# Optimization experiments

Measured on AMD Instinct MI355X. Metric: run time of the kernel, lower is better.

Reference implementation:

```python
import jax, jax.numpy as jnp
import numpy as np

T, B = 128, 64
EMB, HID, NTOK = 400, 1152, 33278
# layer dims: (in, out) per layer, matching AWD_LSTM construction
LAYER_DIMS = [(EMB, HID), (HID, HID), (HID, EMB)]


def _uniform(key, shape, bound):
    return jax.random.uniform(key, shape, jnp.float32, -bound, bound)


def setup_inputs() -> dict:
    key = jax.random.key(0)
    ks = jax.random.split(key, 32)
    inp = {
        "x": jax.random.normal(ks[0], (T, B, EMB), jnp.float32),
        "h0_0": jnp.zeros((B, HID), jnp.float32),
        "h0_1": jnp.zeros((B, HID), jnp.float32),
        "h0_2": jnp.zeros((B, EMB), jnp.float32),
        "c0_0": jnp.zeros((B, HID), jnp.float32),
        "c0_1": jnp.zeros((B, HID), jnp.float32),
        "c0_2": jnp.zeros((B, EMB), jnp.float32),
    }
    ki = 1
    for li, (din, dout) in enumerate(LAYER_DIMS):
        bound = 1.0 / np.sqrt(dout)
        inp[f"W_ih{li}"] = _uniform(ks[ki + 0], (4 * dout, din), bound)
        inp[f"W_hh{li}"] = _uniform(ks[ki + 1], (4 * dout, dout), bound)
        inp[f"b_ih{li}"] = _uniform(ks[ki + 2], (4 * dout,), bound)
        inp[f"b_hh{li}"] = _uniform(ks[ki + 3], (4 * dout,), bound)
        ki += 4
    bd = 1.0 / np.sqrt(EMB)
    inp["W_dec"] = _uniform(ks[ki], (NTOK, EMB), bd)
    inp["b_dec"] = _uniform(ks[ki + 1], (NTOK,), bd)
    return inp


def _lstm_cell(x, h, c, W_ih, W_hh, b_ih, b_hh):
    # PyTorch gate order: i, f, g, o
    gates = x @ W_ih.T + b_ih + h @ W_hh.T + b_hh
    i, f, g, o = jnp.split(gates, 4, axis=-1)
    c_new = jax.nn.sigmoid(f) * c + jax.nn.sigmoid(i) * jnp.tanh(g)
    h_new = jax.nn.sigmoid(o) * jnp.tanh(c_new)
    return h_new, c_new


def reference(x, h0_0, h0_1, h0_2, c0_0, c0_1, c0_2,
              W_ih0, W_hh0, b_ih0, b_hh0,
              W_ih1, W_hh1, b_ih1, b_hh1,
              W_ih2, W_hh2, b_ih2, b_hh2,
              W_dec, b_dec):
    params = [(W_ih0, W_hh0, b_ih0, b_hh0),
              (W_ih1, W_hh1, b_ih1, b_hh1),
              (W_ih2, W_hh2, b_ih2, b_hh2)]

    def step(carry, xt):
        hs, cs = carry
        inp = xt
        new_h, new_c = [], []
        for li in range(3):
            h, c = _lstm_cell(inp, hs[li], cs[li], *params[li])
            new_h.append(h)
            new_c.append(c)
            inp = h
        return (tuple(new_h), tuple(new_c)), new_h[-1]

    carry0 = ((h0_0, h0_1, h0_2), (c0_0, c0_1, c0_2))
    (hs, cs), out = jax.lax.scan(step, carry0, x)  # out: (T, B, EMB)
    decoded = out.reshape(T * B, EMB) @ W_dec.T + b_dec
    return decoded.reshape(T, B, NTOK)
```

## Files before the change

kernel.cpp:

```cpp
#include <hip/hip_runtime.h>
#include <math.h>

typedef unsigned short u16;
typedef __attribute__((ext_vector_type(8))) short short8;
typedef __attribute__((ext_vector_type(4))) float f32x4;
typedef __attribute__((ext_vector_type(2))) float f32x2;

__device__ __forceinline__ u16 f32_to_bf16(float x) {
    union { float f; unsigned int u; } v; v.f = x;
    unsigned int u = v.u;
    return (u16)((u + 0x7FFFu + ((u >> 16) & 1u)) >> 16);
}
__device__ __forceinline__ float bf16_to_f32(u16 h) {
    union { unsigned int u; float f; } v; v.u = ((unsigned int)h) << 16; return v.f;
}

__global__ void split_pad_kernel(const float* __restrict__ src,
                                 u16* __restrict__ hi, u16* __restrict__ lo,
                                 int N, int K, int Npad, int Kpad, int perm)
{
    int idx = blockIdx.x * 256 + threadIdx.x;
    if (idx >= Npad * Kpad) return;
    int n = idx / Kpad, k = idx - n * Kpad;
    float x = 0.f;
    if (n < N && k < K) {
        int srow = n;
        if (perm) { int dout = N >> 2; srow = (n & 3) * dout + (n >> 2); }
        x = src[(size_t)srow * K + k];
    }
    u16 h = f32_to_bf16(x);
    hi[idx] = h;
    lo[idx] = f32_to_bf16(x - bf16_to_f32(h));
}

__global__ void bias_perm_kernel(const float* __restrict__ bi,
                                 const float* __restrict__ bh,
                                 float* __restrict__ out, int N4)
{
    int c = blockIdx.x * 256 + threadIdx.x;
    if (c >= N4) return;
    int dout = N4 >> 2;
    int s = (c & 3) * dout + (c >> 2);
    out[c] = bi[s] + bh[s];
}

__global__ __launch_bounds__(256) void gemm3m(
    const float* __restrict__ Af32,
    const u16* __restrict__ Ahi, const u16* __restrict__ Alo,
    const u16* __restrict__ Whi, const u16* __restrict__ Wlo,
    const float* __restrict__ bias,
    float* __restrict__ C,
    int Nreal, int Kreal, int Kp, int lda, int ldc, int amode,
    int MT, int NSUB)
{
    extern __shared__ __align__(16) char smem[];
    u16 (*As)[128][32] = (u16 (*)[128][32])smem;
    u16 (*Ws)[128][32] = (u16 (*)[128][32])(smem + 16384);
    float (*Cs)[129]   = (float (*)[129])smem;

    const int tid  = threadIdx.x;
    const int lane = tid & 63, wave = tid >> 6;

    const int bid   = blockIdx.x;
    const int super = bid / (NSUB * MT);
    const int rem   = bid - super * (NSUB * MT);
    const int mtile = rem / NSUB;
    const int ntile = super * NSUB + (rem - mtile * NSUB);
    const int m0 = mtile * 128, n0 = ntile * 128;

    const int wm = (wave >> 1) * 64, wn = (wave & 1) * 64;

    f32x4 acc[4][4];
#pragma unroll
    for (int i = 0; i < 4; ++i)
#pragma unroll
        for (int j = 0; j < 4; ++j)
#pragma unroll
            for (int r = 0; r < 4; ++r) acc[i][j][r] = 0.f;

    const int srow = tid >> 2;
    const int sq   = tid & 3;
    const int dq   = (sq ^ ((srow >> 2) & 3)) * 8;
    const int fr   = lane & 15;
    const int fq   = lane >> 4;
    const int rcol = (fq ^ ((fr >> 2) & 3)) * 8;

    for (int k0 = 0; k0 < Kp; k0 += 32) {
#pragma unroll
        for (int half = 0; half < 2; ++half) {
            int row = half * 64 + srow;
            int kc  = k0 + sq * 8;
            if (amode == 0) {
                union { u16 s[8]; short8 v; } uh, ul;
                if (kc + 8 <= Kreal) {
                    const float* p = &Af32[(size_t)(m0 + row) * lda + kc];
#pragma unroll
                    for (int j = 0; j < 8; ++j) {
                        float xv = p[j];
                        u16 hh = f32_to_bf16(xv);
                        uh.s[j] = hh;
                        ul.s[j] = f32_to_bf16(xv - bf16_to_f32(hh));
                    }
                } else {
#pragma unroll
                    for (int j = 0; j < 8; ++j) { uh.s[j] = 0; ul.s[j] = 0; }
                }
                *(short8*)&As[0][row][dq] = uh.v;
                *(short8*)&As[1][row][dq] = ul.v;
            } else {
                size_t ao = (size_t)(m0 + row) * lda + kc;
                *(short8*)&As[0][row][dq] = *(const short8*)(Ahi + ao);
                *(short8*)&As[1][row][dq] = *(const short8*)(Alo + ao);
            }
            size_t wo = (size_t)(n0 + row) * Kp + kc;
            *(short8*)&Ws[0][row][dq] = *(const short8*)(Whi + wo);
            *(short8*)&Ws[1][row][dq] = *(const short8*)(Wlo + wo);
        }
        __syncthreads();

        short8 ah[4], al[4], wh[4], wl[4];
#pragma unroll
        for (int f = 0; f < 4; ++f) {
            int arow = wm + f * 16 + fr;
            ah[f] = *(const short8*)&As[0][arow][rcol];
            al[f] = *(const short8*)&As[1][arow][rcol];
            int wrow = wn + f * 16 + fr;
            wh[f] = *(const short8*)&Ws[0][wrow][rcol];
            wl[f] = *(const short8*)&Ws[1][wrow][rcol];
        }
#pragma unroll
        for (int i = 0; i < 4; ++i)
#pragma unroll
            for (int j = 0; j < 4; ++j) {
                acc[i][j] = __builtin_amdgcn_mfma_f32_16x16x32_bf16(ah[i], wh[j], acc[i][j], 0, 0, 0);
                acc[i][j] = __builtin_amdgcn_mfma_f32_16x16x32_bf16(ah[i], wl[j], acc[i][j], 0, 0, 0);
                acc[i][j] = __builtin_amdgcn_mfma_f32_16x16x32_bf16(al[i], wh[j], acc[i][j], 0, 0, 0);
            }
        __syncthreads();
    }

    const int erow = tid & 31;
    const int echk = tid >> 5;
    const int gm_base = m0 + ((erow >> 4) * 64) + (erow & 15);
    const int gn0 = n0 + echk * 16;
    const bool vec4ok = ((ldc & 3) == 0);

#pragma unroll
    for (int i = 0; i < 4; ++i) {
        __syncthreads();
#pragma unroll
        for (int j = 0; j < 4; ++j)
#pragma unroll
            for (int r = 0; r < 4; ++r)
                Cs[(wave >> 1) * 16 + fq * 4 + r][wn + j * 16 + fr] = acc[i][j][r];
        __syncthreads();

        const int gm = gm_base + i * 16;
        float* crow = C + (size_t)gm * ldc;
        if (gn0 + 16 <= Nreal) {
#pragma unroll
            for (int q = 0; q < 4; ++q) {
                f32x4 v = *(const f32x4*)&Cs[erow][echk * 16 + q * 4];
                if (bias) {
                    f32x4 bv = *(const f32x4*)&bias[gn0 + q * 4];
                    v += bv;
                }
                if (vec4ok) {
                    *(f32x4*)&crow[gn0 + q * 4] = v;
                } else {
                    f32x2 lo2 = {v[0], v[1]}, hi2 = {v[2], v[3]};
                    *(f32x2*)&crow[gn0 + q * 4]     = lo2;
                    *(f32x2*)&crow[gn0 + q * 4 + 2] = hi2;
                }
            }
        } else {
#pragma unroll
            for (int q = 0; q < 4; ++q)
#pragma unroll
                for (int p = 0; p < 4; ++p) {
                    int n = gn0 + q * 4 + p;
                    if (n < Nreal)
                        crow[n] = Cs[erow][echk * 16 + q * 4 + p] + (bias ? bias[n] : 0.f);
                }
        }
    }
}

#define PF(S, KT_) do {                                                        \
    int q_ = (((KT_) * 4 + fq) ^ sxor) * 8;                                    \
    a0h_##S = *(const short8*)&Wlds[rA * Kp + q_];                             \
    a0l_##S = *(const short8*)&Wlds[(32 + rA) * Kp + q_];                      \
    a1h_##S = *(const short8*)&Wlds[rB * Kp + q_];                             \
    a1l_##S = *(const short8*)&Wlds[(32 + rB) * Kp + q_];                      \
    hh_##S = *(const short8*)(hrow_hi + (KT_) * 32 + fq * 8);                  \
    hl_##S = *(const short8*)(hrow_lo + (KT_) * 32 + fq * 8);                  \
} while (0)

#define CM(S) do {                                                             \
    accA = __builtin_amdgcn_mfma_f32_16x16x32_bf16(a0h_##S, hh_##S, accA, 0, 0, 0); \
    accB = __builtin_amdgcn_mfma_f32_16x16x32_bf16(a1h_##S, hh_##S, accB, 0, 0, 0); \
    accA = __builtin_amdgcn_mfma_f32_16x16x32_bf16(a0h_##S, hl_##S, accA, 0, 0, 0); \
    accB = __builtin_amdgcn_mfma_f32_16x16x32_bf16(a1h_##S, hl_##S, accB, 0, 0, 0); \
    accA = __builtin_amdgcn_mfma_f32_16x16x32_bf16(a0l_##S, hh_##S, accA, 0, 0, 0); \
    accB = __builtin_amdgcn_mfma_f32_16x16x32_bf16(a1l_##S, hh_##S, accB, 0, 0, 0); \
} while (0)

__global__ __launch_bounds__(256, 1) void persistent_lstm(
    const u16* __restrict__ Whi, const u16* __restrict__ Wlo,
    const u16* __restrict__ h0hi, const u16* __restrict__ h0lo,
    u16* __restrict__ seqHi, u16* __restrict__ seqLo,
    const float* __restrict__ pre,
    const float* __restrict__ c_in, float* __restrict__ c_out,
    int* __restrict__ gcnt,
    int t0, int N4, int Kp, int dout, int G)
{
    extern __shared__ __align__(16) u16 Wlds[];
    const int tid  = threadIdx.x;
    const int lane = tid & 63, wave = tid >> 6;
    const int fr = lane & 15, fq = lane >> 4;
    const int c0blk = blockIdx.x * 32;
    const int CH = Kp >> 3;
    const int b = wave * 16 + fr;
    const int grp = blockIdx.x & 7;

    for (int idx = tid; idx < 64 * CH; idx += 256) {
        int buf = idx / (32 * CH);
        int rem = idx - buf * 32 * CH;
        int r = rem / CH, q = rem - r * CH;
        const u16* src = buf ? Wlo : Whi;
        short8 v = *(const short8*)(src + (size_t)(c0blk + r) * Kp + q * 8);
        *(short8*)&Wlds[(buf * 32 + r) * Kp + (q ^ (r & 7)) * 8] = v;
    }

    const int cA = c0blk + fq * 4;
    const int cB = cA + 16;
    const int jA = cA >> 2, jB = cB >> 2;
    float cregA = c_in[(size_t)b * dout + jA];
    float cregB = c_in[(size_t)b * dout + jB];

    const int rA = fr, rB = 16 + fr;
    const int sxor = fr & 7;
    const int KT = Kp >> 5;

    f32x4 preA = *(const f32x4*)(pre + (size_t)b * N4 + cA);
    f32x4 preB = *(const f32x4*)(pre + (size_t)b * N4 + cB);
    __syncthreads();

    for (int ts = 0; ts < 64; ++ts) {
        const int t = t0 + ts;
        const u16* hbase_hi = (t == 0) ? h0hi : seqHi + (size_t)(t - 1) * 64 * Kp;
        const u16* hbase_lo = (t == 0) ? h0lo : seqLo + (size_t)(t - 1) * 64 * Kp;
        const u16* hrow_hi = hbase_hi + (size_t)b * Kp;
        const u16* hrow_lo = hbase_lo + (size_t)b * Kp;

        f32x4 accA = {0.f, 0.f, 0.f, 0.f};
        f32x4 accB = {0.f, 0.f, 0.f, 0.f};
        short8 a0h_0, a0l_0, a1h_0, a1l_0, hh_0, hl_0;
        short8 a0h_1, a0l_1, a1h_1, a1l_1, hh_1, hl_1;
        short8 a0h_2, a0l_2, a1h_2, a1l_2, hh_2, hl_2;
        short8 a0h_3, a0l_3, a1h_3, a1l_3, hh_3, hl_3;
        short8 a0h_4, a0l_4, a1h_4, a1l_4, hh_4, hl_4;
        short8 a0h_5, a0l_5, a1h_5, a1l_5, hh_5, hl_5;

        PF(0, 0); PF(1, 1); PF(2, 2); PF(3, 3); PF(4, 4); PF(5, 5);
        for (int kt = 0; kt < KT - 6; kt += 6) {
            CM(0); PF(0, kt + 6);
            CM(1); PF(1, kt + 7);
            CM(2); PF(2, kt + 8);
            CM(3); PF(3, kt + 9);
            CM(4); PF(4, kt + 10);
            CM(5); PF(5, kt + 11);
        }
        CM(0); CM(1); CM(2); CM(3); CM(4); CM(5);

#pragma unroll
        for (int ct = 0; ct < 2; ++ct) {
            f32x4 a = ct ? accB : accA;
            f32x4 p = ct ? preB : preA;
            int j  = ct ? jB : jA;
            float gi = a[0] + p[0];
            float gf = a[1] + p[1];
            float gg = a[2] + p[2];
            float go_ = a[3] + p[3];
            float si = 1.f / (1.f + expf(-gi));
            float sf = 1.f / (1.f + expf(-gf));
            float so = 1.f / (1.f + expf(-go_));
            float tg = tanhf(gg);
            float cn = sf * (ct ? cregB : cregA) + si * tg;
            float hv = so * tanhf(cn);
            if (ct) cregB = cn; else cregA = cn;
            u16 hb = f32_to_bf16(hv);
            size_t so_ = (size_t)(t * 64 + b) * Kp + j;
            seqHi[so_] = hb;
            seqLo[so_] = f32_to_bf16(hv - bf16_to_f32(hb));
        }

        if (ts != 63) {
            __syncthreads();
            {
                const float* prow2 = pre + (size_t)((ts + 1) * 64 + b) * N4;
                preA = *(const f32x4*)(prow2 + cA);
                preB = *(const f32x4*)(prow2 + cB);
            }
            if (tid == 0) {
                __builtin_amdgcn_fence(__ATOMIC_RELEASE, "agent");
                __hip_atomic_fetch_add(&gcnt[(ts * 8 + grp) * 32], 1,
                                       __ATOMIC_RELAXED, __HIP_MEMORY_SCOPE_AGENT);
                int sum;
                do {
                    sum = 0;
#pragma unroll
                    for (int g = 0; g < 8; ++g)
                        sum += __hip_atomic_load(&gcnt[(ts * 8 + g) * 32],
                                                 __ATOMIC_RELAXED, __HIP_MEMORY_SCOPE_AGENT);
                    if (sum < G) __builtin_amdgcn_s_sleep(1);
                } while (sum < G);
            }
            __syncthreads();
            __builtin_amdgcn_sched_barrier(0);
        }
    }

    c_out[(size_t)b * dout + jA] = cregA;
    c_out[(size_t)b * dout + jB] = cregB;
}

extern "C" void kernel_launch(void* const* d_in, const int* in_sizes, int n_in,
                              void* d_out, int out_size, void* d_ws, size_t ws_size,
                              hipStream_t stream)
{
    const int T = 128, B = 64, EMB = 400, HID = 1152, NTOK = 33278;
    const int TB = T * B;

    const float* x     = (const float*)d_in[0];
    const float* h0[3] = {(const float*)d_in[1], (const float*)d_in[2], (const float*)d_in[3]};
    const float* c0[3] = {(const float*)d_in[4], (const float*)d_in[5], (const float*)d_in[6]};
    const float* W_ih[3] = {(const float*)d_in[7],  (const float*)d_in[11], (const float*)d_in[15]};
    const float* W_hh[3] = {(const float*)d_in[8],  (const float*)d_in[12], (const float*)d_in[16]};
    const float* b_ih[3] = {(const float*)d_in[9],  (const float*)d_in[13], (const float*)d_in[17]};
    const float* b_hh[3] = {(const float*)d_in[10], (const float*)d_in[14], (const float*)d_in[18]};
    const float* W_dec = (const float*)d_in[19];
    const float* b_dec = (const float*)d_in[20];

    const int din[3]    = {EMB, HID, HID};
    const int Kpre[3]   = {416, 1152, 1152};
    const int dh[3]     = {HID, HID, EMB};
    const int KpH[3]    = {1152, 1152, 576};
    const int N4[3]     = {4608, 4608, 1600};
    const int N4p128[3] = {4608, 4608, 1664};
    const int NSUBpre[3] = {6, 6, 13};
    const int Gp[3]     = {144, 144, 50};

    char* wsp = (char*)d_ws;
    size_t off = 0;
    auto alloc = [&](size_t bytes) -> char* {
        char* p = wsp + off; off = (off + bytes + 255) & ~(size_t)255; return p;
    };

    float* pre   = (float*)alloc((size_t)4096 * 4608 * 4);
    u16* seqHi   = (u16*)alloc((size_t)TB * 1152 * 2);
    u16* seqLo   = (u16*)alloc((size_t)TB * 1152 * 2);
    u16* WihHi   = (u16*)alloc((size_t)4608 * 1152 * 2);
    u16* WihLo   = (u16*)alloc((size_t)4608 * 1152 * 2);
    u16* WhhHi   = (u16*)alloc((size_t)4608 * 1152 * 2);
    u16* WhhLo   = (u16*)alloc((size_t)4608 * 1152 * 2);
    u16* h0Hi    = (u16*)alloc((size_t)B * 1152 * 2);
    u16* h0Lo    = (u16*)alloc((size_t)B * 1152 * 2);
    float* bsum  = (float*)alloc(4608 * 4);
    float* cstb  = (float*)alloc((size_t)B * HID * 4);
    const size_t gcntN = (size_t)6 * 64 * 8 * 32;
    int* gcnt = (int*)alloc(gcntN * 4);
    u16* WdecHi  = (u16*)pre;
    u16* WdecLo  = (u16*)pre + (size_t)33280 * 416;

    hipMemsetAsync(gcnt, 0, gcntN * 4, stream);
    hipFuncSetAttribute(reinterpret_cast<const void*>(persistent_lstm),
                        hipFuncAttributeMaxDynamicSharedMemorySize, 160 * 1024);
    hipFuncSetAttribute(reinterpret_cast<const void*>(gemm3m),
                        hipFuncAttributeMaxDynamicSharedMemorySize, 64 * 1024);

    auto run_split = [&](const float* src, u16* hi, u16* lo,
                         int N, int K, int Npad, int Kpad, int perm) {
        int total = Npad * Kpad;
        split_pad_kernel<<<(total + 255) / 256, 256, 0, stream>>>(
            src, hi, lo, N, K, Npad, Kpad, perm);
    };

    for (int l = 0; l < 3; ++l) {
        run_split(W_hh[l], WhhHi, WhhLo, N4[l], dh[l], N4[l], KpH[l], 1);
        run_split(h0[l], h0Hi, h0Lo, B, dh[l], B, KpH[l], 0);
        run_split(W_ih[l], WihHi, WihLo, N4[l], din[l], N4p128[l], Kpre[l], 1);
        bias_perm_kernel<<<(N4[l] + 255) / 256, 256, 0, stream>>>(
            b_ih[l], b_hh[l], bsum, N4[l]);

        const int ldaA = (l == 0) ? EMB : KpH[l - 1];
        const int NT = N4p128[l] / 128, MT = 32;
        const size_t ldsB = (size_t)128 * KpH[l];

        for (int halfT = 0; halfT < 2; ++halfT) {
            const int li = l * 2 + halfT;
            const float* Af32 = (l == 0) ? (x + (size_t)halfT * 4096 * EMB) : nullptr;
            const u16* Ah = (l == 0) ? nullptr : (seqHi + (size_t)halfT * 4096 * ldaA);
            const u16* Al = (l == 0) ? nullptr : (seqLo + (size_t)halfT * 4096 * ldaA);
            gemm3m<<<dim3(NT * MT), 256, 32768, stream>>>(
                Af32, Ah, Al, WihHi, WihLo, bsum, pre,
                N4[l], din[l], Kpre[l], ldaA, N4[l], (l == 0) ? 0 : 1,
                MT, NSUBpre[l]);

            const float* cin = (halfT == 0) ? c0[l] : cstb;
            persistent_lstm<<<dim3(Gp[l]), 256, ldsB, stream>>>(
                WhhHi, WhhLo, h0Hi, h0Lo, seqHi, seqLo, pre,
                cin, cstb,
                gcnt + (size_t)li * 64 * 8 * 32,
                halfT * 64, N4[l], KpH[l], dh[l], Gp[l]);
        }
    }

    run_split(W_dec, WdecHi, WdecLo, NTOK, EMB, 33280, 416, 0);
    gemm3m<<<dim3(260 * 64), 256, 32768, stream>>>(
        nullptr, seqHi, seqLo, WdecHi, WdecLo, b_dec, (float*)d_out,
        NTOK, EMB, 416, 576, NTOK, 1,
        64, 5);
}
```

Baseline: 6.536 ms.

## Run full-sequence LSTM per layer with flag barrier and async LDS loads in GEMM

Replaces the two half-sequence GEMM+persistent-LSTM launches per layer with a single full-T input GEMM and one persistent kernel running all timesteps. The grid barrier changes from grouped atomic counters to per-block monotonic flags that each thread polls. The GEMM uses direct global-to-LDS loads for bf16 operands and a new tile-order mapping. The aim is fewer launches, cheaper inter-block synchronization and less register staging, but the pre buffer grows to the full sequence, and the new block mapping assumes 64 M-tiles.

```diff
diff --git a/kernel.cpp b/kernel.cpp
--- a/kernel.cpp
+++ b/kernel.cpp
@@ -2,6 +2,7 @@
 #include <math.h>
 
 typedef unsigned short u16;
+typedef unsigned int u32;
 typedef __attribute__((ext_vector_type(8))) short short8;
 typedef __attribute__((ext_vector_type(4))) float f32x4;
 typedef __attribute__((ext_vector_type(2))) float f32x2;
@@ -13,6 +14,12 @@
 }
 __device__ __forceinline__ float bf16_to_f32(u16 h) {
     union { unsigned int u; float f; } v; v.u = ((unsigned int)h) << 16; return v.f;
+}
+
+__device__ __forceinline__ void gload16(const u16* g, u16* l) {
+    __builtin_amdgcn_global_load_lds(
+        (const __attribute__((address_space(1))) void*)g,
+        (__attribute__((address_space(3))) void*)l, 16, 0, 0);
 }
 
 __global__ void split_pad_kernel(const float* __restrict__ src,
@@ -50,8 +57,7 @@
     const u16* __restrict__ Whi, const u16* __restrict__ Wlo,
     const float* __restrict__ bias,
     float* __restrict__ C,
-    int Nreal, int Kreal, int Kp, int lda, int ldc, int amode,
-    int MT, int NSUB)
+    int Nreal, int Kreal, int Kp, int lda, int ldc, int amode)
 {
     extern __shared__ __align__(16) char smem[];
     u16 (*As)[128][32] = (u16 (*)[128][32])smem;
@@ -62,10 +68,10 @@
     const int lane = tid & 63, wave = tid >> 6;
 
     const int bid   = blockIdx.x;
-    const int super = bid / (NSUB * MT);
-    const int rem   = bid - super * (NSUB * MT);
-    const int mtile = rem / NSUB;
-    const int ntile = super * NSUB + (rem - mtile * NSUB);
+    const int chunk = bid & 7;
+    const int c     = bid >> 3;
+    const int ntile = c >> 3;
+    const int mtile = (chunk << 3) | (c & 7);
     const int m0 = mtile * 128, n0 = ntile * 128;
 
     const int wm = (wave >> 1) * 64, wn = (wave & 1) * 64;
@@ -85,12 +91,23 @@
     const int fq   = lane >> 4;
     const int rcol = (fq ^ ((fr >> 2) & 3)) * 8;
 
+    const u16* gb = nullptr; u16* lb = nullptr; int gstr = 0;
+    if (amode != 0) {
+        u16* AsB = (u16*)smem;
+        u16* WsB = (u16*)(smem + 16384);
+        if (wave == 0)      { gb = Ahi + (size_t)m0 * lda; gstr = lda; lb = AsB; }
+        else if (wave == 1) { gb = Alo + (size_t)m0 * lda; gstr = lda; lb = AsB + 4096; }
+        else if (wave == 2) { gb = Whi + (size_t)n0 * Kp;  gstr = Kp;  lb = WsB; }
+        else                { gb = Wlo + (size_t)n0 * Kp;  gstr = Kp;  lb = WsB + 4096; }
+    }
+    const int lrow = lane >> 2, lq = lane & 3;
+
     for (int k0 = 0; k0 < Kp; k0 += 32) {
-#pragma unroll
-        for (int half = 0; half < 2; ++half) {
-            int row = half * 64 + srow;
-            int kc  = k0 + sq * 8;
-            if (amode == 0) {
+        if (amode == 0) {
+#pragma unroll
+            for (int half = 0; half < 2; ++half) {
+                int row = half * 64 + srow;
+                int kc  = k0 + sq * 8;
                 union { u16 s[8]; short8 v; } uh, ul;
                 if (kc + 8 <= Kreal) {
                     const float* p = &Af32[(size_t)(m0 + row) * lda + kc];
@@ -107,14 +124,17 @@
                 }
                 *(short8*)&As[0][row][dq] = uh.v;
                 *(short8*)&As[1][row][dq] = ul.v;
-            } else {
-                size_t ao = (size_t)(m0 + row) * lda + kc;
-                *(short8*)&As[0][row][dq] = *(const short8*)(Ahi + ao);
-                *(short8*)&As[1][row][dq] = *(const short8*)(Alo + ao);
-            }
-            size_t wo = (size_t)(n0 + row) * Kp + kc;
-            *(short8*)&Ws[0][row][dq] = *(const short8*)(Whi + wo);
-            *(short8*)&Ws[1][row][dq] = *(const short8*)(Wlo + wo);
+                size_t wo = (size_t)(n0 + row) * Kp + k0 + sq * 8;
+                *(short8*)&Ws[0][row][dq] = *(const short8*)(Whi + wo);
+                *(short8*)&Ws[1][row][dq] = *(const short8*)(Wlo + wo);
+            }
+        } else {
+#pragma unroll
+            for (int g = 0; g < 8; ++g) {
+                int row = g * 16 + lrow;
+                int srcq = lq ^ ((row >> 2) & 3);
+                gload16(gb + (size_t)row * gstr + k0 + srcq * 8, lb + g * 512);
+            }
         }
         __syncthreads();
 
@@ -211,8 +231,8 @@
     u16* __restrict__ seqHi, u16* __restrict__ seqLo,
     const float* __restrict__ pre,
     const float* __restrict__ c_in, float* __restrict__ c_out,
-    int* __restrict__ gcnt,
-    int t0, int N4, int Kp, int dout, int G)
+    int* __restrict__ flags,
+    int N4, int Kp, int dout, int G, int TSTEPS)
 {
     extern __shared__ __align__(16) u16 Wlds[];
     const int tid  = threadIdx.x;
@@ -221,7 +241,6 @@
     const int c0blk = blockIdx.x * 32;
     const int CH = Kp >> 3;
     const int b = wave * 16 + fr;
-    const int grp = blockIdx.x & 7;
 
     for (int idx = tid; idx < 64 * CH; idx += 256) {
         int buf = idx / (32 * CH);
@@ -246,10 +265,9 @@
     f32x4 preB = *(const f32x4*)(pre + (size_t)b * N4 + cB);
     __syncthreads();
 
-    for (int ts = 0; ts < 64; ++ts) {
-        const int t = t0 + ts;
-        const u16* hbase_hi = (t == 0) ? h0hi : seqHi + (size_t)(t - 1) * 64 * Kp;
-        const u16* hbase_lo = (t == 0) ? h0lo : seqLo + (size_t)(t - 1) * 64 * Kp;
+    for (int ts = 0; ts < TSTEPS; ++ts) {
+        const u16* hbase_hi = (ts == 0) ? h0hi : seqHi + (size_t)(ts - 1) * 64 * Kp;
+        const u16* hbase_lo = (ts == 0) ? h0lo : seqLo + (size_t)(ts - 1) * 64 * Kp;
         const u16* hrow_hi = hbase_hi + (size_t)b * Kp;
         const u16* hrow_lo = hbase_lo + (size_t)b * Kp;
 
@@ -290,31 +308,27 @@
             float hv = so * tanhf(cn);
             if (ct) cregB = cn; else cregA = cn;
             u16 hb = f32_to_bf16(hv);
-            size_t so_ = (size_t)(t * 64 + b) * Kp + j;
+            size_t so_ = (size_t)(ts * 64 + b) * Kp + j;
             seqHi[so_] = hb;
             seqLo[so_] = f32_to_bf16(hv - bf16_to_f32(hb));
         }
 
-        if (ts != 63) {
+        if (ts != TSTEPS - 1) {
             __syncthreads();
+            if (tid == 0) {
+                __builtin_amdgcn_fence(__ATOMIC_RELEASE, "agent");
+                __hip_atomic_store(&flags[blockIdx.x], ts + 1,
+                                   __ATOMIC_RELAXED, __HIP_MEMORY_SCOPE_AGENT);
+            }
             {
                 const float* prow2 = pre + (size_t)((ts + 1) * 64 + b) * N4;
                 preA = *(const f32x4*)(prow2 + cA);
                 preB = *(const f32x4*)(prow2 + cB);
             }
-            if (tid == 0) {
-                __builtin_amdgcn_fence(__ATOMIC_RELEASE, "agent");
-                __hip_atomic_fetch_add(&gcnt[(ts * 8 + grp) * 32], 1,
-                                       __ATOMIC_RELAXED, __HIP_MEMORY_SCOPE_AGENT);
-                int sum;
-                do {
-                    sum = 0;
-#pragma unroll
-                    for (int g = 0; g < 8; ++g)
-                        sum += __hip_atomic_load(&gcnt[(ts * 8 + g) * 32],
-                                                 __ATOMIC_RELAXED, __HIP_MEMORY_SCOPE_AGENT);
-                    if (sum < G) __builtin_amdgcn_s_sleep(1);
-                } while (sum < G);
+            if (tid < G) {
+                while (__hip_atomic_load(&flags[tid], __ATOMIC_RELAXED,
+                                         __HIP_MEMORY_SCOPE_AGENT) < ts + 1)
+                    __builtin_amdgcn_s_sleep(1);
             }
             __syncthreads();
             __builtin_amdgcn_sched_barrier(0);
@@ -348,7 +362,6 @@
     const int KpH[3]    = {1152, 1152, 576};
     const int N4[3]     = {4608, 4608, 1600};
     const int N4p128[3] = {4608, 4608, 1664};
-    const int NSUBpre[3] = {6, 6, 13};
     const int Gp[3]     = {144, 144, 50};
 
     char* wsp = (char*)d_ws;
@@ -357,7 +370,7 @@
         char* p = wsp + off; off = (off + bytes + 255) & ~(size_t)255; return p;
     };
 
-    float* pre   = (float*)alloc((size_t)4096 * 4608 * 4);
+    float* pre   = (float*)alloc((size_t)TB * 4608 * 4);
     u16* seqHi   = (u16*)alloc((size_t)TB * 1152 * 2);
     u16* seqLo   = (u16*)alloc((size_t)TB * 1152 * 2);
     u16* WihHi   = (u16*)alloc((size_t)4608 * 1152 * 2);
@@ -368,12 +381,11 @@
     u16* h0Lo    = (u16*)alloc((size_t)B * 1152 * 2);
     float* bsum  = (float*)alloc(4608 * 4);
     float* cstb  = (float*)alloc((size_t)B * HID * 4);
-    const size_t gcntN = (size_t)6 * 64 * 8 * 32;
-    int* gcnt = (int*)alloc(gcntN * 4);
+    int* flags   = (int*)alloc(3 * 256 * 4);
     u16* WdecHi  = (u16*)pre;
     u16* WdecLo  = (u16*)pre + (size_t)33280 * 416;
 
-    hipMemsetAsync(gcnt, 0, gcntN * 4, stream);
+    hipMemsetAsync(flags, 0, 3 * 256 * 4, stream);
     hipFuncSetAttribute(reinterpret_cast<const void*>(persistent_lstm),
                         hipFuncAttributeMaxDynamicSharedMemorySize, 160 * 1024);
     hipFuncSetAttribute(reinterpret_cast<const void*>(gemm3m),
@@ -394,31 +406,24 @@
             b_ih[l], b_hh[l], bsum, N4[l]);
 
         const int ldaA = (l == 0) ? EMB : KpH[l - 1];
-        const int NT = N4p128[l] / 128, MT = 32;
+        const int NT = N4p128[l] / 128;
         const size_t ldsB = (size_t)128 * KpH[l];
 
-        for (int halfT = 0; halfT < 2; ++halfT) {
-            const int li = l * 2 + halfT;
-            const float* Af32 = (l == 0) ? (x + (size_t)halfT * 4096 * EMB) : nullptr;
-            const u16* Ah = (l == 0) ? nullptr : (seqHi + (size_t)halfT * 4096 * ldaA);
-            const u16* Al = (l == 0) ? nullptr : (seqLo + (size_t)halfT * 4096 * ldaA);
-            gemm3m<<<dim3(NT * MT), 256, 32768, stream>>>(
-                Af32, Ah, Al, WihHi, WihLo, bsum, pre,
-                N4[l], din[l], Kpre[l], ldaA, N4[l], (l == 0) ? 0 : 1,
-                MT, NSUBpre[l]);
-
-            const float* cin = (halfT == 0) ? c0[l] : cstb;
-            persistent_lstm<<<dim3(Gp[l]), 256, ldsB, stream>>>(
-                WhhHi, WhhLo, h0Hi, h0Lo, seqHi, seqLo, pre,
-                cin, cstb,
-                gcnt + (size_t)li * 64 * 8 * 32,
-                halfT * 64, N4[l], KpH[l], dh[l], Gp[l]);
-        }
+        const float* Af32 = (l == 0) ? x : nullptr;
+        const u16* Ah = (l == 0) ? nullptr : seqHi;
+        const u16* Al = (l == 0) ? nullptr : seqLo;
+        gemm3m<<<dim3(NT * 64), 256, 32768, stream>>>(
+            Af32, Ah, Al, WihHi, WihLo, bsum, pre,
+            N4[l], din[l], Kpre[l], ldaA, N4[l], (l == 0) ? 0 : 1);
+
+        persistent_lstm<<<dim3(Gp[l]), 256, ldsB, stream>>>(
+            WhhHi, WhhLo, h0Hi, h0Lo, seqHi, seqLo, pre,
+            c0[l], cstb, flags + l * 256,
+            N4[l], KpH[l], dh[l], Gp[l], T);
     }
 
     run_split(W_dec, WdecHi, WdecLo, NTOK, EMB, 33280, 416, 0);
     gemm3m<<<dim3(260 * 64), 256, 32768, stream>>>(
         nullptr, seqHi, seqLo, WdecHi, WdecLo, b_dec, (float*)d_out,
-        NTOK, EMB, 416, 576, NTOK, 1,
-        64, 5);
-}
+        NTOK, EMB, 416, 576, NTOK, 1);
+}
```

Result: slower. 6.754 ms (+3.3%).
